# Kernel optimization log

Measured on AMD Instinct MI355X. Metric: run time of the kernel, lower is better.

## Reference

```python
import jax, jax.numpy as jnp
import numpy as np

N = 50000      # nodes
E = 800000     # edges
F_IN = 128     # input_dim
H = 4          # GAT heads
C = 32         # hidden_dim (per head)
HC = H * C     # 128, concat GAT output
NG = 64        # graphs in batch
OUT = 10       # classes


def _gat_conv(x, src, dst, W, att_src, att_dst, bias):
    # PyG GATConv (concat=True, add_self_loops=True, negative_slope=0.2)
    n = x.shape[0]
    h = (x @ W).reshape(n, H, -1)                      # [N,H,C]
    a_s = (h * att_src).sum(-1)                        # [N,H]
    a_d = (h * att_dst).sum(-1)                        # [N,H]
    loop = jnp.arange(n)
    s = jnp.concatenate([src, loop])                   # self-loops appended
    d = jnp.concatenate([dst, loop])
    e = jax.nn.leaky_relu(a_s[s] + a_d[d], 0.2)        # [E+N,H]
    m = jax.ops.segment_max(e, d, num_segments=n)
    e = jnp.exp(e - m[d])
    z = jax.ops.segment_sum(e, d, num_segments=n)
    alpha = e / (z[d] + 1e-16)                         # edge softmax per dst,head
    out = jax.ops.segment_sum(h[s] * alpha[..., None], d, num_segments=n)
    return out.reshape(n, -1) + bias                   # [N,H*C]


def setup_inputs() -> dict:
    key = jax.random.key(0)
    ks = jax.random.split(key, 20)
    g = lambda k, shp, fan: jax.random.normal(k, shp, jnp.float32) / np.sqrt(fan)
    inp = {
        'x': jax.random.normal(ks[0], (N, F_IN), jnp.float32),
        'edge_index': jax.random.randint(ks[1], (2, E), 0, N),
        'batch': jnp.sort(jax.random.randint(ks[2], (N,), 0, NG)),
        # GATConv 1: F_IN -> H*C
        'W1': g(ks[3], (F_IN, HC), F_IN),
        'as1': g(ks[4], (H, C), C), 'ad1': g(ks[5], (H, C), C),
        'b1': jnp.zeros((HC,), jnp.float32),
        # GATConv 2: H*C -> H*C
        'W2': g(ks[6], (HC, HC), HC),
        'as2': g(ks[7], (H, C), C), 'ad2': g(ks[8], (H, C), C),
        'b2': jnp.zeros((HC,), jnp.float32),
        # GraphConv: H*C -> C  (lin_rel has bias, lin_root does not)
        'W3r': g(ks[9], (HC, C), HC), 'W3l': g(ks[10], (HC, C), HC),
        'b3': jnp.zeros((C,), jnp.float32),
        # SAGEConv: C -> C (mean aggr; lin_l has bias, lin_r does not)
        'W4l': g(ks[11], (C, C), C), 'b4l': jnp.zeros((C,), jnp.float32),
        'W4r': g(ks[12], (C, C), C),
        # MLP head
        'Wf1': g(ks[13], (C, C), C), 'bf1': jnp.zeros((C,), jnp.float32),
        'Wf2': g(ks[14], (C, OUT), C), 'bf2': jnp.zeros((OUT,), jnp.float32),
    }
    return inp


def reference(x, edge_index, batch, W1, as1, ad1, b1, W2, as2, ad2, b2,
              W3r, W3l, b3, W4l, b4l, W4r, Wf1, bf1, Wf2, bf2):
    src, dst = edge_index[0], edge_index[1]
    relu = jax.nn.relu
    n = x.shape[0]
    # GAT layers (dropout is identity in eval)
    x = relu(_gat_conv(x, src, dst, W1, as1, ad1, b1))
    x = relu(_gat_conv(x, src, dst, W2, as2, ad2, b2))
    # GraphConv: lin_rel(sum_neighbors) + lin_root(x)
    agg = jax.ops.segment_sum(x[src], dst, num_segments=n)
    x = relu(agg @ W3r + b3 + x @ W3l)
    # SAGEConv: lin_l(mean_neighbors) + lin_r(x)
    deg = jax.ops.segment_sum(jnp.ones((src.shape[0],), x.dtype), dst, num_segments=n)
    mean = jax.ops.segment_sum(x[src], dst, num_segments=n) / jnp.maximum(deg, 1.0)[:, None]
    x = relu(mean @ W4l + b4l + x @ W4r)
    # global mean pool over graphs
    cnt = jax.ops.segment_sum(jnp.ones((n,), x.dtype), batch, num_segments=NG)
    gpool = jax.ops.segment_sum(x, batch, num_segments=NG) / jnp.maximum(cnt, 1.0)[:, None]
    gpool = relu(gpool @ Wf1 + bf1)
    return gpool @ Wf2 + bf2
```

## Files before the change

### kernel.cpp

```cpp
#include <hip/hip_runtime.h>
#include <hip/hip_bf16.h>
#include <type_traits>


typedef __bf16 v8bf __attribute__((ext_vector_type(8)));
typedef float  v4f  __attribute__((ext_vector_type(4)));

__device__ __forceinline__ float lrelu(float x) { return x > 0.f ? x : 0.2f * x; }

__device__ __forceinline__ unsigned short f2bf(float f) {
    unsigned u = __float_as_uint(f);
    unsigned r = (u + 0x7FFF + ((u >> 16) & 1)) >> 16;
    return (unsigned short)r;
}
__device__ __forceinline__ float bfbits2f(unsigned short u) {
    return __uint_as_float((unsigned)u << 16);
}
__device__ __forceinline__ float bflo(int v) { return __uint_as_float((unsigned)v << 16); }
__device__ __forceinline__ float bfhi(int v) { return __uint_as_float((unsigned)v & 0xffff0000u); }
__device__ __forceinline__ int packbf2(float a, float b) {
    return (int)f2bf(a) | ((int)f2bf(b) << 16);
}

__device__ __forceinline__ void fma8(float* acc, int4 u, float w) {
    acc[0] += w * bflo(u.x); acc[1] += w * bfhi(u.x);
    acc[2] += w * bflo(u.y); acc[3] += w * bfhi(u.y);
    acc[4] += w * bflo(u.z); acc[5] += w * bfhi(u.z);
    acc[6] += w * bflo(u.w); acc[7] += w * bfhi(u.w);
}


__global__ __launch_bounds__(256) void bucket_hist(const int* __restrict__ dst,
                                                   int* __restrict__ bcount,
                                                   int E, int nbuck) {
    __shared__ int hist[256];
    int t = threadIdx.x;
    for (int i = t; i < nbuck; i += 256) hist[i] = 0;
    __syncthreads();
    int base = blockIdx.x * 4096;
    #pragma unroll
    for (int k = 0; k < 16; ++k) {
        int e = base + k * 256 + t;
        if (e < E) atomicAdd(&hist[dst[e] >> 8], 1);
    }
    __syncthreads();
    for (int i = t; i < nbuck; i += 256) {
        int c = hist[i];
        if (c) atomicAdd(&bcount[i], c);
    }
}

__global__ __launch_bounds__(256) void scan_convert(
    const int* __restrict__ bcount, int* __restrict__ bbase, int* __restrict__ gcursor,
    int nbuck, int E, int* __restrict__ rowptr, int n,
    const float* __restrict__ W1, const float* __restrict__ W2,
    const float* __restrict__ W3r, const float* __restrict__ W3l,
    const float* __restrict__ as1, const float* __restrict__ ad1,
    const float* __restrict__ as2, const float* __restrict__ ad2,
    __hip_bfloat16* __restrict__ W1t, __hip_bfloat16* __restrict__ W2t,
    __hip_bfloat16* __restrict__ W3rt, __hip_bfloat16* __restrict__ W3lt)
{
    int t = threadIdx.x;
    if (blockIdx.x == 0) {
        __shared__ int red[256];
        int v = (t < nbuck) ? bcount[t] : 0;
        red[t] = v;
        __syncthreads();
        for (int off = 1; off < 256; off <<= 1) {
            int u = (t >= off) ? red[t - off] : 0;
            __syncthreads();
            red[t] += u;
            __syncthreads();
        }
        int ex = red[t] - v;
        if (t < nbuck) { bbase[t] = ex; gcursor[t] = ex; }
        if (t == 0) { bbase[nbuck] = E; rowptr[n] = E; }
        return;
    }
    int b = blockIdx.x - 1;
    int i = b * 256 + t;
    {
        int k = i >> 7, c = i & 127;
        *(unsigned short*)&W1t[c * 128 + k] = f2bf(W1[i]);
        *(unsigned short*)&W2t[c * 128 + k] = f2bf(W2[i]);
    }
    if (i < 4096) {
        int k = i >> 5, c = i & 31;
        *(unsigned short*)&W3rt[c * 128 + k] = f2bf(W3r[i]);
        *(unsigned short*)&W3lt[c * 128 + k] = f2bf(W3l[i]);
    }
    if (b == 0) {
        for (int u = t; u < 512; u += 256) {
            int k = u & 127, hd = u >> 7;
            float vs1 = 0.f, vd1 = 0.f, vs2 = 0.f, vd2 = 0.f;
            #pragma unroll
            for (int j = 0; j < 32; ++j) {
                int c = hd * 32 + j;
                float w1 = W1[k * 128 + c], w2 = W2[k * 128 + c];
                vs1 += w1 * as1[c]; vd1 += w1 * ad1[c];
                vs2 += w2 * as2[c]; vd2 += w2 * ad2[c];
            }
            unsigned short h1s = f2bf(vs1), h1d = f2bf(vd1);
            unsigned short h2s = f2bf(vs2), h2d = f2bf(vd2);
            *(unsigned short*)&W1t[(128 + hd) * 128 + k] = h1s;
            *(unsigned short*)&W1t[(132 + hd) * 128 + k] = f2bf(vs1 - bfbits2f(h1s));
            *(unsigned short*)&W1t[(136 + hd) * 128 + k] = h1d;
            *(unsigned short*)&W1t[(140 + hd) * 128 + k] = f2bf(vd1 - bfbits2f(h1d));
            *(unsigned short*)&W2t[(128 + hd) * 128 + k] = h2s;
            *(unsigned short*)&W2t[(132 + hd) * 128 + k] = f2bf(vs2 - bfbits2f(h2s));
            *(unsigned short*)&W2t[(136 + hd) * 128 + k] = h2d;
            *(unsigned short*)&W2t[(140 + hd) * 128 + k] = f2bf(vd2 - bfbits2f(h2d));
        }
    }
}

__global__ __launch_bounds__(256) void bucket_scatter(const int* __restrict__ dst,
                                                      const int* __restrict__ src,
                                                      int* __restrict__ gcursor,
                                                      int* __restrict__ pairs,
                                                      int E, int nbuck) {
    __shared__ int hist[256], lcur[256];
    int t = threadIdx.x;
    for (int i = t; i < nbuck; i += 256) hist[i] = 0;
    __syncthreads();
    int base = blockIdx.x * 2048;
    int dreg[8];
    #pragma unroll
    for (int k = 0; k < 8; ++k) {
        int e = base + k * 256 + t;
        int d = (e < E) ? dst[e] : -1;
        dreg[k] = d;
        if (d >= 0) atomicAdd(&hist[d >> 8], 1);
    }
    __syncthreads();
    for (int i = t; i < nbuck; i += 256) {
        int c = hist[i];
        lcur[i] = c ? atomicAdd(&gcursor[i], c) : 0;
    }
    __syncthreads();
    #pragma unroll
    for (int k = 0; k < 8; ++k) {
        int e = base + k * 256 + t;
        if (e < E) {
            int d = dreg[k];
            int p = atomicAdd(&lcur[d >> 8], 1);
            pairs[p] = ((d & 255) << 17) | src[e];
        }
    }
}

__global__ __launch_bounds__(256) void bucket_fill(const int* __restrict__ pairs,
                                                   const int* __restrict__ bbase,
                                                   int* __restrict__ rowptr,
                                                   int* __restrict__ colsrc, int n) {
    __shared__ int deg[256], excl[256], cur[256];
    int b = blockIdx.x, t = threadIdx.x;
    int e0 = bbase[b], e1 = bbase[b + 1];
    int d0 = b << 8;
    deg[t] = 0;
    __syncthreads();
    for (int j = e0 + t; j < e1; j += 256)
        atomicAdd(&deg[pairs[j] >> 17], 1);
    __syncthreads();
    int v = deg[t];
    excl[t] = v;
    __syncthreads();
    for (int off = 1; off < 256; off <<= 1) {
        int u = (t >= off) ? excl[t - off] : 0;
        __syncthreads();
        excl[t] += u;
        __syncthreads();
    }
    int base = e0 + excl[t] - v;
    if (d0 + t < n) rowptr[d0 + t] = base;
    cur[t] = base;
    __syncthreads();
    for (int j = e0 + t; j < e1; j += 256) {
        int w = pairs[j];
        int p = atomicAdd(&cur[w >> 17], 1);
        colsrc[p] = w & 0x1FFFF;
    }
}

template <typename T>
__global__ __launch_bounds__(256) void gemm_att_mfma(
    const T* __restrict__ X, const __hip_bfloat16* __restrict__ Wt,
    __hip_bfloat16* __restrict__ h, float* __restrict__ a_s, float* __restrict__ a_d, int n)
{
    __shared__ __align__(16) __hip_bfloat16 sWt[144 * 136];
    int t = threadIdx.x;
    for (int i = t; i < 144 * 16; i += 256) {
        int row = i >> 4, chh = i & 15;
        *(int4*)&sWt[row * 136 + chh * 8] = *(const int4*)&Wt[row * 128 + chh * 8];
    }
    __syncthreads();
    int wave = t >> 6, lane = t & 63, quad = lane >> 4, l16 = lane & 15;

    v8bf z;
    #pragma unroll
    for (int i = 0; i < 8; ++i) z[i] = (__bf16)0.f;

    int nrb = (n + 15) >> 4;
    for (int rb = blockIdx.x * 4 + wave; rb < nrb; rb += gridDim.x * 4) {
        int rowbase = rb * 16;
        int arow = rowbase + l16;
        bool ok = arow < n;
        v8bf af[4];
        if constexpr (std::is_same<T, float>::value) {
            const float* xf = X + (size_t)(ok ? arow : 0) * 128;
            #pragma unroll
            for (int ks = 0; ks < 4; ++ks) {
                if (ok) {
                    float4 u = *(const float4*)&xf[ks * 32 + quad * 8];
                    float4 v = *(const float4*)&xf[ks * 32 + quad * 8 + 4];
                    v8bf a;
                    unsigned short r;
                    r = f2bf(u.x); a[0] = *(__bf16*)&r;
                    r = f2bf(u.y); a[1] = *(__bf16*)&r;
                    r = f2bf(u.z); a[2] = *(__bf16*)&r;
                    r = f2bf(u.w); a[3] = *(__bf16*)&r;
                    r = f2bf(v.x); a[4] = *(__bf16*)&r;
                    r = f2bf(v.y); a[5] = *(__bf16*)&r;
                    r = f2bf(v.z); a[6] = *(__bf16*)&r;
                    r = f2bf(v.w); a[7] = *(__bf16*)&r;
                    af[ks] = a;
                } else af[ks] = z;
            }
        } else {
            const v8bf* px = (const v8bf*)(X + (size_t)(ok ? arow : 0) * 128);
            #pragma unroll
            for (int ks = 0; ks < 4; ++ks) af[ks] = ok ? px[ks * 4 + quad] : z;
        }

        v4f acc[9];
        #pragma unroll
        for (int ct = 0; ct < 9; ++ct) acc[ct] = (v4f){0.f, 0.f, 0.f, 0.f};
        #pragma unroll
        for (int ct = 0; ct < 9; ++ct) {
            #pragma unroll
            for (int ks = 0; ks < 4; ++ks) {
                v8bf b = *(const v8bf*)&sWt[(ct * 16 + l16) * 136 + ks * 32 + quad * 8];
                acc[ct] = __builtin_amdgcn_mfma_f32_16x16x32_bf16(af[ks], b, acc[ct], 0, 0, 0);
            }
        }

        #pragma unroll
        for (int reg = 0; reg < 4; ++reg) {
            int r = rowbase + quad * 4 + reg;
            if (r < n) {
                #pragma unroll
                for (int ct = 0; ct < 8; ++ct)
                    *(unsigned short*)&h[(size_t)r * 128 + ct * 16 + l16] = f2bf(acc[ct][reg]);
            }
        }
        #pragma unroll
        for (int reg = 0; reg < 4; ++reg) {
            float v = acc[8][reg] + __shfl_xor(acc[8][reg], 4);
            int r = rowbase + quad * 4 + reg;
            if (r < n) {
                if (l16 < 4)                    a_s[r * 4 + l16] = v;
                else if (l16 >= 8 && l16 < 12)  a_d[r * 4 + (l16 - 8)] = v;
            }
        }
    }
}

__global__ __launch_bounds__(256) void gat_aggr(
    const __hip_bfloat16* __restrict__ h, const float* __restrict__ a_s,
    const float* __restrict__ a_d,
    const int* __restrict__ rowptr, const int* __restrict__ colsrc,
    const float* __restrict__ bias, __hip_bfloat16* __restrict__ out, int n)
{
    __shared__ float s_w[4][2 * 32 * 4];
    int t = threadIdx.x;
    int wave = t >> 6, lane = t & 63;
    int half = lane >> 5, hl = lane & 31;
    int d = blockIdx.x * 8 + wave * 2 + half;
    if (d >= n) d = n - 1;
    int beg = rowptr[d], end = rowptr[d + 1];
    int cnt = end - beg;
    int cmax = max(cnt, __shfl_xor(cnt, 32));
    float4 ad4 = *(const float4*)&a_d[d * 4];
    float4 asd = *(const float4*)&a_s[d * 4];
    float es0 = lrelu(asd.x + ad4.x), es1 = lrelu(asd.y + ad4.y);
    float es2 = lrelu(asd.z + ad4.z), es3 = lrelu(asd.w + ad4.w);

    int egrp = hl >> 4, l16 = hl & 15;
    int ch = l16 * 8;
    int head = l16 >> 2;
    const char* hb = (const char*)h;
    unsigned chb = (unsigned)(ch << 1);
    int sbase = half * 128;
    int lbase = half * 32;

    float acc[8];
    #pragma unroll
    for (int i = 0; i < 8; ++i) acc[i] = 0.f;
    float zp = 0.f;

    for (int j0 = 0; j0 < cmax; j0 += 32) {
        int ne = cnt - j0;
        float w0 = 0.f, w1 = 0.f, w2 = 0.f, w3 = 0.f;
        int s = 0;
        if (hl < ne) {
            s = colsrc[beg + j0 + hl];
            float4 sv = *(const float4*)&a_s[s * 4];
            w0 = __expf(lrelu(sv.x + ad4.x));
            w1 = __expf(lrelu(sv.y + ad4.y));
            w2 = __expf(lrelu(sv.z + ad4.z));
            w3 = __expf(lrelu(sv.w + ad4.w));
        }
        float4 wv = {w0, w1, w2, w3};
        *(float4*)&s_w[wave][sbase + hl * 4] = wv;
        __asm volatile("s_waitcnt lgkmcnt(0)" ::: "memory");
        int nemax = cmax - j0; if (nemax > 32) nemax = 32;
        int kmax = (nemax + 1) >> 1;
        int k = 0;
        for (; k + 4 <= kmax; k += 4) {
            int jb = egrp + 2 * k;
            int ss0 = __shfl(s, lbase + jb);
            int ss1 = __shfl(s, lbase + jb + 2);
            int ss2 = __shfl(s, lbase + jb + 4);
            int ss3 = __shfl(s, lbase + jb + 6);
            float wj0 = s_w[wave][sbase + jb * 4 + head];
            float wj1 = s_w[wave][sbase + (jb + 2) * 4 + head];
            float wj2 = s_w[wave][sbase + (jb + 4) * 4 + head];
            float wj3 = s_w[wave][sbase + (jb + 6) * 4 + head];
            int4 u0 = *(const int4*)(hb + (((unsigned)ss0 << 8) + chb));
            int4 u1 = *(const int4*)(hb + (((unsigned)ss1 << 8) + chb));
            int4 u2 = *(const int4*)(hb + (((unsigned)ss2 << 8) + chb));
            int4 u3 = *(const int4*)(hb + (((unsigned)ss3 << 8) + chb));
            zp += (wj0 + wj1) + (wj2 + wj3);
            fma8(acc, u0, wj0);
            fma8(acc, u1, wj1);
            fma8(acc, u2, wj2);
            fma8(acc, u3, wj3);
        }
        for (; k + 2 <= kmax; k += 2) {
            int jb = egrp + 2 * k;
            int ss0 = __shfl(s, lbase + jb);
            int ss1 = __shfl(s, lbase + jb + 2);
            float wj0 = s_w[wave][sbase + jb * 4 + head];
            float wj1 = s_w[wave][sbase + (jb + 2) * 4 + head];
            int4 u0 = *(const int4*)(hb + (((unsigned)ss0 << 8) + chb));
            int4 u1 = *(const int4*)(hb + (((unsigned)ss1 << 8) + chb));
            zp += wj0 + wj1;
            fma8(acc, u0, wj0);
            fma8(acc, u1, wj1);
        }
        if (k < kmax) {
            int jb = egrp + 2 * k;
            int ss0 = __shfl(s, lbase + jb);
            float wj0 = s_w[wave][sbase + jb * 4 + head];
            int4 u0 = *(const int4*)(hb + (((unsigned)ss0 << 8) + chb));
            zp += wj0;
            fma8(acc, u0, wj0);
        }
    }

    int4 hu = {0, 0, 0, 0};
    float4 b0 = {0.f, 0.f, 0.f, 0.f}, b1 = {0.f, 0.f, 0.f, 0.f};
    if (egrp == 0) {
        hu = *(const int4*)(hb + (((unsigned)d << 8) + chb));
        b0 = *(const float4*)&bias[ch];
        b1 = *(const float4*)&bias[ch + 4];
    }
    zp += __shfl_xor(zp, 16);
    #pragma unroll
    for (int i = 0; i < 8; ++i) acc[i] += __shfl_xor(acc[i], 16);

    if (egrp == 0) {
        float eh = (head < 2) ? (head == 0 ? es0 : es1) : (head == 2 ? es2 : es3);
        float ws = __expf(eh);
        float inv = 1.f / (zp + ws + 1e-16f);
        float hs[8] = {bflo(hu.x), bfhi(hu.x), bflo(hu.y), bfhi(hu.y),
                       bflo(hu.z), bfhi(hu.z), bflo(hu.w), bfhi(hu.w)};
        float o[8];
        o[0] = fmaxf((acc[0] + ws * hs[0]) * inv + b0.x, 0.f);
        o[1] = fmaxf((acc[1] + ws * hs[1]) * inv + b0.y, 0.f);
        o[2] = fmaxf((acc[2] + ws * hs[2]) * inv + b0.z, 0.f);
        o[3] = fmaxf((acc[3] + ws * hs[3]) * inv + b0.w, 0.f);
        o[4] = fmaxf((acc[4] + ws * hs[4]) * inv + b1.x, 0.f);
        o[5] = fmaxf((acc[5] + ws * hs[5]) * inv + b1.y, 0.f);
        o[6] = fmaxf((acc[6] + ws * hs[6]) * inv + b1.z, 0.f);
        o[7] = fmaxf((acc[7] + ws * hs[7]) * inv + b1.w, 0.f);
        int4 ou;
        ou.x = packbf2(o[0], o[1]); ou.y = packbf2(o[2], o[3]);
        ou.z = packbf2(o[4], o[5]); ou.w = packbf2(o[6], o[7]);
        *(int4*)&out[(size_t)d * 128 + ch] = ou;
    }
}

__global__ __launch_bounds__(256) void graphconv_lin(
    const __hip_bfloat16* __restrict__ Xb,
    const __hip_bfloat16* __restrict__ Wrt, const __hip_bfloat16* __restrict__ Wlt,
    const float* __restrict__ bias, __hip_bfloat16* __restrict__ y,
    float* __restrict__ root, int n)
{
    __shared__ __align__(16) __hip_bfloat16 sWr[32 * 136], sWl[32 * 136];
    int t = threadIdx.x;
    for (int i = t; i < 32 * 16; i += 256) {
        int row = i >> 4, chh = i & 15;
        *(int4*)&sWr[row * 136 + chh * 8] = *(const int4*)&Wrt[row * 128 + chh * 8];
        *(int4*)&sWl[row * 136 + chh * 8] = *(const int4*)&Wlt[row * 128 + chh * 8];
    }
    __syncthreads();
    int wave = t >> 6, lane = t & 63, quad = lane >> 4, l16 = lane & 15;

    v8bf z;
    #pragma unroll
    for (int i = 0; i < 8; ++i) z[i] = (__bf16)0.f;

    int nrb = (n + 15) >> 4;
    for (int rb = blockIdx.x * 4 + wave; rb < nrb; rb += gridDim.x * 4) {
        int rowbase = rb * 16;
        int arow = rowbase + l16;
        bool ok = arow < n;
        const v8bf* px = (const v8bf*)(Xb + (size_t)(ok ? arow : 0) * 128);
        v8bf fx[4];
        #pragma unroll
        for (int ks = 0; ks < 4; ++ks) fx[ks] = ok ? px[ks * 4 + quad] : z;

        v4f accR[2], accL[2];
        #pragma unroll
        for (int ct = 0; ct < 2; ++ct) {
            accR[ct] = (v4f){0.f, 0.f, 0.f, 0.f};
            accL[ct] = (v4f){0.f, 0.f, 0.f, 0.f};
            #pragma unroll
            for (int ks = 0; ks < 4; ++ks) {
                v8bf br = *(const v8bf*)&sWr[(ct * 16 + l16) * 136 + ks * 32 + quad * 8];
                accR[ct] = __builtin_amdgcn_mfma_f32_16x16x32_bf16(fx[ks], br, accR[ct], 0, 0, 0);
                v8bf bl = *(const v8bf*)&sWl[(ct * 16 + l16) * 136 + ks * 32 + quad * 8];
                accL[ct] = __builtin_amdgcn_mfma_f32_16x16x32_bf16(fx[ks], bl, accL[ct], 0, 0, 0);
            }
        }
        #pragma unroll
        for (int ct = 0; ct < 2; ++ct) {
            float bcol = bias[ct * 16 + l16];
            #pragma unroll
            for (int reg = 0; reg < 4; ++reg) {
                int r = rowbase + quad * 4 + reg;
                if (r < n) {
                    *(unsigned short*)&y[(size_t)r * 32 + ct * 16 + l16] = f2bf(accR[ct][reg]);
                    root[(size_t)r * 32 + ct * 16 + l16] = accL[ct][reg] + bcol;
                }
            }
        }
    }
}

__global__ __launch_bounds__(256) void graphconv_aggr(
    const __hip_bfloat16* __restrict__ y, const float* __restrict__ root,
    const int* __restrict__ rowptr, const int* __restrict__ colsrc,
    __hip_bfloat16* __restrict__ x3, int n)
{
    int t = threadIdx.x;
    int wave = t >> 6, lane = t & 63;
    int qr = lane >> 4, hl = lane & 15;
    int d = blockIdx.x * 16 + wave * 4 + qr;
    if (d >= n) d = n - 1;
    int beg = rowptr[d];
    int cnt = rowptr[d + 1] - beg;
    int cm = max(cnt, __shfl_xor(cnt, 16));
    cm = max(cm, __shfl_xor(cm, 32));
    int l4 = hl & 3, egrp = hl >> 2;
    int ch = l4 * 8;
    int lbase = qr * 16;
    float acc[8];
    #pragma unroll
    for (int i = 0; i < 8; ++i) acc[i] = 0.f;
    for (int j0 = 0; j0 < cm; j0 += 16) {
        int ne = cnt - j0;
        int s = (hl < ne) ? colsrc[beg + j0 + hl] : 0;
        int nemax = cm - j0; if (nemax > 16) nemax = 16;
        int kmax = (nemax + 3) >> 2;
        int k = 0;
        for (; k + 2 <= kmax; k += 2) {
            int ja = egrp + 4 * k, jb = ja + 4;
            int sa = __shfl(s, lbase + ja);
            int sb = __shfl(s, lbase + jb);
            float ma = (ja < ne) ? 1.f : 0.f;
            float mb = (jb < ne) ? 1.f : 0.f;
            int4 ua = *(const int4*)&y[(size_t)sa * 32 + ch];
            int4 ub = *(const int4*)&y[(size_t)sb * 32 + ch];
            fma8(acc, ua, ma);
            fma8(acc, ub, mb);
        }
        if (k < kmax) {
            int ja = egrp + 4 * k;
            int sa = __shfl(s, lbase + ja);
            float ma = (ja < ne) ? 1.f : 0.f;
            int4 ua = *(const int4*)&y[(size_t)sa * 32 + ch];
            fma8(acc, ua, ma);
        }
    }
    float4 r0 = {0.f, 0.f, 0.f, 0.f}, r1 = {0.f, 0.f, 0.f, 0.f};
    if (egrp == 0) {
        r0 = *(const float4*)&root[(size_t)d * 32 + ch];
        r1 = *(const float4*)&root[(size_t)d * 32 + ch + 4];
    }
    #pragma unroll
    for (int off = 4; off < 16; off <<= 1)
        #pragma unroll
        for (int i = 0; i < 8; ++i) acc[i] += __shfl_xor(acc[i], off);
    if (egrp == 0) {
        float o[8];
        o[0] = fmaxf(acc[0] + r0.x, 0.f); o[1] = fmaxf(acc[1] + r0.y, 0.f);
        o[2] = fmaxf(acc[2] + r0.z, 0.f); o[3] = fmaxf(acc[3] + r0.w, 0.f);
        o[4] = fmaxf(acc[4] + r1.x, 0.f); o[5] = fmaxf(acc[5] + r1.y, 0.f);
        o[6] = fmaxf(acc[6] + r1.z, 0.f); o[7] = fmaxf(acc[7] + r1.w, 0.f);
        int4 ou;
        ou.x = packbf2(o[0], o[1]); ou.y = packbf2(o[2], o[3]);
        ou.z = packbf2(o[4], o[5]); ou.w = packbf2(o[6], o[7]);
        *(int4*)&x3[(size_t)d * 32 + ch] = ou;
    }
}

__global__ __launch_bounds__(256) void mean_aggr32(
    const __hip_bfloat16* __restrict__ x, const int* __restrict__ rowptr,
    const int* __restrict__ colsrc, float* __restrict__ mean, int n)
{
    int t = threadIdx.x;
    int wave = t >> 6, lane = t & 63;
    int qr = lane >> 4, hl = lane & 15;
    int d = blockIdx.x * 16 + wave * 4 + qr;
    if (d >= n) d = n - 1;
    int beg = rowptr[d];
    int cnt = rowptr[d + 1] - beg;
    int cm = max(cnt, __shfl_xor(cnt, 16));
    cm = max(cm, __shfl_xor(cm, 32));
    int l4 = hl & 3, egrp = hl >> 2;
    int ch = l4 * 8;
    int lbase = qr * 16;
    float acc[8];
    #pragma unroll
    for (int i = 0; i < 8; ++i) acc[i] = 0.f;
    for (int j0 = 0; j0 < cm; j0 += 16) {
        int ne = cnt - j0;
        int s = (hl < ne) ? colsrc[beg + j0 + hl] : 0;
        int nemax = cm - j0; if (nemax > 16) nemax = 16;
        int kmax = (nemax + 3) >> 2;
        int k = 0;
        for (; k + 2 <= kmax; k += 2) {
            int ja = egrp + 4 * k, jb = ja + 4;
            int sa = __shfl(s, lbase + ja);
            int sb = __shfl(s, lbase + jb);
            float ma = (ja < ne) ? 1.f : 0.f;
            float mb = (jb < ne) ? 1.f : 0.f;
            int4 ua = *(const int4*)&x[(size_t)sa * 32 + ch];
            int4 ub = *(const int4*)&x[(size_t)sb * 32 + ch];
            fma8(acc, ua, ma);
            fma8(acc, ub, mb);
        }
        if (k < kmax) {
            int ja = egrp + 4 * k;
            int sa = __shfl(s, lbase + ja);
            float ma = (ja < ne) ? 1.f : 0.f;
            int4 ua = *(const int4*)&x[(size_t)sa * 32 + ch];
            fma8(acc, ua, ma);
        }
    }
    #pragma unroll
    for (int off = 4; off < 16; off <<= 1)
        #pragma unroll
        for (int i = 0; i < 8; ++i) acc[i] += __shfl_xor(acc[i], off);
    if (egrp == 0) {
        float invd = 1.f / fmaxf((float)cnt, 1.f);
        float4 lo = {acc[0] * invd, acc[1] * invd, acc[2] * invd, acc[3] * invd};
        float4 hi = {acc[4] * invd, acc[5] * invd, acc[6] * invd, acc[7] * invd};
        *(float4*)&mean[(size_t)d * 32 + ch]     = lo;
        *(float4*)&mean[(size_t)d * 32 + ch + 4] = hi;
    }
}

__global__ __launch_bounds__(256) void sage_gemm(
    const float* __restrict__ mean, const __hip_bfloat16* __restrict__ xin,
    const float* __restrict__ Wl, const float* __restrict__ bl,
    const float* __restrict__ Wr, float* __restrict__ out, int n)
{
    __shared__ __align__(16) float sWl[32 * 32], sWr[32 * 32];
    __shared__ __align__(16) float sm[8 * 32], sx[8 * 32];
    int t = threadIdx.x;
    for (int i = t; i < 1024; i += 256) { sWl[i] = Wl[i]; sWr[i] = Wr[i]; }
    int c = t & 31, rr = t >> 5;
    float bc = bl[c];
    for (int row0 = blockIdx.x * 8; row0 < n; row0 += gridDim.x * 8) {
        __syncthreads();
        {
            int i = t;
            int r = i >> 5, cc = i & 31;
            int row = row0 + r;
            sm[i] = (row < n) ? mean[row * 32 + cc] : 0.f;
            sx[i] = (row < n) ? bfbits2f(*(const unsigned short*)&xin[row * 32 + cc]) : 0.f;
        }
        __syncthreads();
        float acc = bc;
        const float4* pm = (const float4*)&sm[rr * 32];
        const float4* px = (const float4*)&sx[rr * 32];
        #pragma unroll
        for (int k4 = 0; k4 < 8; ++k4) {
            float4 vm = pm[k4], vx = px[k4];
            const float* wl = &sWl[(k4 * 4) * 32 + c];
            const float* wr = &sWr[(k4 * 4) * 32 + c];
            acc += vm.x * wl[0] + vm.y * wl[32] + vm.z * wl[64] + vm.w * wl[96];
            acc += vx.x * wr[0] + vx.y * wr[32] + vx.z * wr[64] + vx.w * wr[96];
        }
        int row = row0 + rr;
        if (row < n) out[row * 32 + c] = fmaxf(acc, 0.f);
    }
}

__device__ __forceinline__ int lower_bound_i(const int* a, int n, int key) {
    int lo = 0, hi = n;
    while (lo < hi) { int mid = (lo + hi) >> 1; if (a[mid] < key) lo = mid + 1; else hi = mid; }
    return lo;
}

__global__ __launch_bounds__(256) void pool_kernel(
    const float* __restrict__ x, const int* __restrict__ batch,
    float* __restrict__ gpool, int n)
{
    int g = blockIdx.x;
    int lo = lower_bound_i(batch, n, g);
    int hi = lower_bound_i(batch, n, g + 1);
    int t = threadIdx.x;
    int c = t & 31, rr = t >> 5;
    float acc = 0.f;
    for (int i = lo + rr; i < hi; i += 8) acc += x[i * 32 + c];
    __shared__ float sred[256];
    sred[t] = acc;
    __syncthreads();
    if (t < 128) sred[t] += sred[t + 128];
    __syncthreads();
    if (t < 64) sred[t] += sred[t + 64];
    __syncthreads();
    if (t < 32) {
        float v = sred[t] + sred[t + 32];
        gpool[g * 32 + t] = v / fmaxf((float)(hi - lo), 1.f);
    }
}

__global__ __launch_bounds__(256) void head_kernel(
    const float* __restrict__ gpool, const float* __restrict__ Wf1, const float* __restrict__ bf1,
    const float* __restrict__ Wf2, const float* __restrict__ bf2, float* __restrict__ out)
{
    __shared__ float sg[64 * 32], st[64 * 32];
    __shared__ float sW1[32 * 32], sW2[32 * 10];
    int t = threadIdx.x;
    for (int i = t; i < 2048; i += 256) sg[i] = gpool[i];
    for (int i = t; i < 1024; i += 256) sW1[i] = Wf1[i];
    for (int i = t; i < 320; i += 256) sW2[i] = Wf2[i];
    __syncthreads();
    for (int i = t; i < 2048; i += 256) {
        int g = i >> 5, c = i & 31;
        float acc = bf1[c];
        #pragma unroll
        for (int k = 0; k < 32; ++k) acc += sg[g * 32 + k] * sW1[k * 32 + c];
        st[i] = fmaxf(acc, 0.f);
    }
    __syncthreads();
    for (int i = t; i < 640; i += 256) {
        int g = i / 10, o = i - g * 10;
        float acc = bf2[o];
        #pragma unroll
        for (int k = 0; k < 32; ++k) acc += st[g * 32 + k] * sW2[k * 10 + o];
        out[i] = acc;
    }
}

extern "C" void kernel_launch(void* const* d_in, const int* in_sizes, int n_in,
                              void* d_out, int out_size, void* d_ws, size_t ws_size,
                              hipStream_t stream) {
    const float* x    = (const float*)d_in[0];
    const int*   ei   = (const int*)d_in[1];
    const int*   batch= (const int*)d_in[2];
    const float* W1   = (const float*)d_in[3];
    const float* as1  = (const float*)d_in[4];
    const float* ad1  = (const float*)d_in[5];
    const float* b1   = (const float*)d_in[6];
    const float* W2   = (const float*)d_in[7];
    const float* as2  = (const float*)d_in[8];
    const float* ad2  = (const float*)d_in[9];
    const float* b2   = (const float*)d_in[10];
    const float* W3r  = (const float*)d_in[11];
    const float* W3l  = (const float*)d_in[12];
    const float* b3   = (const float*)d_in[13];
    const float* W4l  = (const float*)d_in[14];
    const float* b4l  = (const float*)d_in[15];
    const float* W4r  = (const float*)d_in[16];
    const float* Wf1  = (const float*)d_in[17];
    const float* bf1  = (const float*)d_in[18];
    const float* Wf2  = (const float*)d_in[19];
    const float* bf2  = (const float*)d_in[20];

    const int N = in_sizes[0] / 128;
    const int E = in_sizes[1] / 2;
    const int* src = ei;
    const int* dst = ei + E;

    char* p = (char*)d_ws;
    auto alloc = [&](size_t bytes) -> void* {
        void* r = (void*)p;
        p += (bytes + 255) & ~(size_t)255;
        return r;
    };
    __hip_bfloat16* buf1 = (__hip_bfloat16*)alloc((size_t)N * 128 * 2);
    __hip_bfloat16* buf2 = (__hip_bfloat16*)alloc((size_t)N * 128 * 2);
    __hip_bfloat16* buf3 = (__hip_bfloat16*)alloc((size_t)N * 128 * 2);
    float* aS     = (float*)alloc((size_t)N * 4 * 4);
    float* aD     = (float*)alloc((size_t)N * 4 * 4);
    int*   rowptr = (int*)alloc((size_t)(N + 1) * 4);
    int*   colsrc = (int*)alloc((size_t)E * 4);
    int*   bcount = (int*)alloc(256 * 4);
    int*   bbase  = (int*)alloc(257 * 4);
    int*   gcursor= (int*)alloc(256 * 4);
    __hip_bfloat16* W1t  = (__hip_bfloat16*)alloc(144 * 128 * 2);
    __hip_bfloat16* W2t  = (__hip_bfloat16*)alloc(144 * 128 * 2);
    __hip_bfloat16* W3rt = (__hip_bfloat16*)alloc(32 * 128 * 2);
    __hip_bfloat16* W3lt = (__hip_bfloat16*)alloc(32 * 128 * 2);
    float* gpool  = (float*)alloc(64 * 32 * 4);

    __hip_bfloat16* X3b  = buf2;
    float*          MEAN = (float*)((char*)buf2 + (((size_t)N * 32 * 2 + 255) & ~(size_t)255));
    float*          X4   = (float*)buf1;
    __hip_bfloat16* Y32  = buf3;
    float*          ROOT = (float*)((char*)buf3 + (((size_t)N * 32 * 2 + 255) & ~(size_t)255));
    int*            pairs = (int*)buf3;

    const int nbuck = (N + 255) >> 8;

    hipMemsetAsync(bcount, 0, 256 * 4, stream);
    bucket_hist<<<(E + 4095) / 4096, 256, 0, stream>>>(dst, bcount, E, nbuck);
    scan_convert<<<65, 256, 0, stream>>>(bcount, bbase, gcursor, nbuck, E, rowptr, N,
                                         W1, W2, W3r, W3l, as1, ad1, as2, ad2,
                                         W1t, W2t, W3rt, W3lt);
    bucket_scatter<<<(E + 2047) / 2048, 256, 0, stream>>>(dst, src, gcursor, pairs, E, nbuck);
    bucket_fill<<<nbuck, 256, 0, stream>>>(pairs, bbase, rowptr, colsrc, N);

    int gmm = (N + 63) / 64;
    if (gmm > 320) gmm = 320;
    const int gag2 = (N + 7) / 8;
    const int gag4 = (N + 15) / 16;
    gemm_att_mfma<float><<<gmm, 256, 0, stream>>>(x, W1t, buf3, aS, aD, N);
    gat_aggr<<<gag2, 256, 0, stream>>>(buf3, aS, aD, rowptr, colsrc, b1, buf2, N);
    gemm_att_mfma<__hip_bfloat16><<<gmm, 256, 0, stream>>>(buf2, W2t, buf3, aS, aD, N);
    gat_aggr<<<gag2, 256, 0, stream>>>(buf3, aS, aD, rowptr, colsrc, b2, buf1, N);
    graphconv_lin<<<gmm, 256, 0, stream>>>(buf1, W3rt, W3lt, b3, Y32, ROOT, N);
    graphconv_aggr<<<gag4, 256, 0, stream>>>(Y32, ROOT, rowptr, colsrc, X3b, N);
    mean_aggr32<<<gag4, 256, 0, stream>>>(X3b, rowptr, colsrc, MEAN, N);
    sage_gemm<<<1024, 256, 0, stream>>>(MEAN, X3b, W4l, b4l, W4r, X4, N);
    pool_kernel<<<64, 256, 0, stream>>>(X4, batch, gpool, N);
    head_kernel<<<1, 256, 0, stream>>>(gpool, Wf1, bf1, Wf2, bf2, (float*)d_out);
}
```

Measured before the change: 328.9 us.

## Narrow per-node lane groups in GAT and 32-wide aggregation kernels

The GAT aggregation now gives each destination node 16 lanes instead of 32, so one wave handles four nodes and there is no cross-group reduction at the end. The graphconv and mean aggregation kernels give each node 8 lanes instead of 16, so one wave handles eight nodes with a single shuffle reduction. Both changes aim to cut idle lanes and shuffle-reduction overhead on low-degree nodes (average degree about 16). In exchange, each lane serialises more edges per node, so there is less memory-level parallelism per node and more divergence from degree imbalance within a wave.

```diff
diff --git a/kernel.cpp b/kernel.cpp
--- a/kernel.cpp
+++ b/kernel.cpp
@@ -271,39 +271,37 @@
     const int* __restrict__ rowptr, const int* __restrict__ colsrc,
     const float* __restrict__ bias, __hip_bfloat16* __restrict__ out, int n)
 {
-    __shared__ float s_w[4][2 * 32 * 4];
+    __shared__ float s_w[4][4 * 16 * 4];
     int t = threadIdx.x;
     int wave = t >> 6, lane = t & 63;
-    int half = lane >> 5, hl = lane & 31;
-    int d = blockIdx.x * 8 + wave * 2 + half;
+    int q = lane >> 4, l16 = lane & 15;
+    int d = blockIdx.x * 16 + wave * 4 + q;
     if (d >= n) d = n - 1;
-    int beg = rowptr[d], end = rowptr[d + 1];
-    int cnt = end - beg;
-    int cmax = max(cnt, __shfl_xor(cnt, 32));
+    int beg = rowptr[d];
+    int cnt = rowptr[d + 1] - beg;
+    int cm = max(cnt, __shfl_xor(cnt, 16));
+    cm = max(cm, __shfl_xor(cm, 32));
     float4 ad4 = *(const float4*)&a_d[d * 4];
     float4 asd = *(const float4*)&a_s[d * 4];
-    float es0 = lrelu(asd.x + ad4.x), es1 = lrelu(asd.y + ad4.y);
-    float es2 = lrelu(asd.z + ad4.z), es3 = lrelu(asd.w + ad4.w);
-
-    int egrp = hl >> 4, l16 = hl & 15;
+
     int ch = l16 * 8;
     int head = l16 >> 2;
     const char* hb = (const char*)h;
     unsigned chb = (unsigned)(ch << 1);
-    int sbase = half * 128;
-    int lbase = half * 32;
+    int sbase = q * 64;
+    int lbase = q * 16;
 
     float acc[8];
     #pragma unroll
     for (int i = 0; i < 8; ++i) acc[i] = 0.f;
     float zp = 0.f;
 
-    for (int j0 = 0; j0 < cmax; j0 += 32) {
+    for (int j0 = 0; j0 < cm; j0 += 16) {
         int ne = cnt - j0;
         float w0 = 0.f, w1 = 0.f, w2 = 0.f, w3 = 0.f;
         int s = 0;
-        if (hl < ne) {
-            s = colsrc[beg + j0 + hl];
+        if (l16 < ne) {
+            s = colsrc[beg + j0 + l16];
             float4 sv = *(const float4*)&a_s[s * 4];
             w0 = __expf(lrelu(sv.x + ad4.x));
             w1 = __expf(lrelu(sv.y + ad4.y));
@@ -311,21 +309,19 @@
             w3 = __expf(lrelu(sv.w + ad4.w));
         }
         float4 wv = {w0, w1, w2, w3};
-        *(float4*)&s_w[wave][sbase + hl * 4] = wv;
+        *(float4*)&s_w[wave][sbase + l16 * 4] = wv;
         __asm volatile("s_waitcnt lgkmcnt(0)" ::: "memory");
-        int nemax = cmax - j0; if (nemax > 32) nemax = 32;
-        int kmax = (nemax + 1) >> 1;
+        int nemax = cm - j0; if (nemax > 16) nemax = 16;
         int k = 0;
-        for (; k + 4 <= kmax; k += 4) {
-            int jb = egrp + 2 * k;
-            int ss0 = __shfl(s, lbase + jb);
-            int ss1 = __shfl(s, lbase + jb + 2);
-            int ss2 = __shfl(s, lbase + jb + 4);
-            int ss3 = __shfl(s, lbase + jb + 6);
-            float wj0 = s_w[wave][sbase + jb * 4 + head];
-            float wj1 = s_w[wave][sbase + (jb + 2) * 4 + head];
-            float wj2 = s_w[wave][sbase + (jb + 4) * 4 + head];
-            float wj3 = s_w[wave][sbase + (jb + 6) * 4 + head];
+        for (; k + 4 <= nemax; k += 4) {
+            int ss0 = __shfl(s, lbase + k);
+            int ss1 = __shfl(s, lbase + k + 1);
+            int ss2 = __shfl(s, lbase + k + 2);
+            int ss3 = __shfl(s, lbase + k + 3);
+            float wj0 = s_w[wave][sbase + k * 4 + head];
+            float wj1 = s_w[wave][sbase + (k + 1) * 4 + head];
+            float wj2 = s_w[wave][sbase + (k + 2) * 4 + head];
+            float wj3 = s_w[wave][sbase + (k + 3) * 4 + head];
             int4 u0 = *(const int4*)(hb + (((unsigned)ss0 << 8) + chb));
             int4 u1 = *(const int4*)(hb + (((unsigned)ss1 << 8) + chb));
             int4 u2 = *(const int4*)(hb + (((unsigned)ss2 << 8) + chb));
@@ -336,59 +332,38 @@
             fma8(acc, u2, wj2);
             fma8(acc, u3, wj3);
         }
-        for (; k + 2 <= kmax; k += 2) {
-            int jb = egrp + 2 * k;
-            int ss0 = __shfl(s, lbase + jb);
-            int ss1 = __shfl(s, lbase + jb + 2);
-            float wj0 = s_w[wave][sbase + jb * 4 + head];
-            float wj1 = s_w[wave][sbase + (jb + 2) * 4 + head];
-            int4 u0 = *(const int4*)(hb + (((unsigned)ss0 << 8) + chb));
-            int4 u1 = *(const int4*)(hb + (((unsigned)ss1 << 8) + chb));
-            zp += wj0 + wj1;
-            fma8(acc, u0, wj0);
-            fma8(acc, u1, wj1);
-        }
-        if (k < kmax) {
-            int jb = egrp + 2 * k;
-            int ss0 = __shfl(s, lbase + jb);
-            float wj0 = s_w[wave][sbase + jb * 4 + head];
+        for (; k < nemax; ++k) {
+            int ss0 = __shfl(s, lbase + k);
+            float wj0 = s_w[wave][sbase + k * 4 + head];
             int4 u0 = *(const int4*)(hb + (((unsigned)ss0 << 8) + chb));
             zp += wj0;
             fma8(acc, u0, wj0);
         }
     }
 
-    int4 hu = {0, 0, 0, 0};
-    float4 b0 = {0.f, 0.f, 0.f, 0.f}, b1 = {0.f, 0.f, 0.f, 0.f};
-    if (egrp == 0) {
-        hu = *(const int4*)(hb + (((unsigned)d << 8) + chb));
-        b0 = *(const float4*)&bias[ch];
-        b1 = *(const float4*)&bias[ch + 4];
-    }
-    zp += __shfl_xor(zp, 16);
-    #pragma unroll
-    for (int i = 0; i < 8; ++i) acc[i] += __shfl_xor(acc[i], 16);
-
-    if (egrp == 0) {
-        float eh = (head < 2) ? (head == 0 ? es0 : es1) : (head == 2 ? es2 : es3);
-        float ws = __expf(eh);
-        float inv = 1.f / (zp + ws + 1e-16f);
-        float hs[8] = {bflo(hu.x), bfhi(hu.x), bflo(hu.y), bfhi(hu.y),
-                       bflo(hu.z), bfhi(hu.z), bflo(hu.w), bfhi(hu.w)};
-        float o[8];
-        o[0] = fmaxf((acc[0] + ws * hs[0]) * inv + b0.x, 0.f);
-        o[1] = fmaxf((acc[1] + ws * hs[1]) * inv + b0.y, 0.f);
-        o[2] = fmaxf((acc[2] + ws * hs[2]) * inv + b0.z, 0.f);
-        o[3] = fmaxf((acc[3] + ws * hs[3]) * inv + b0.w, 0.f);
-        o[4] = fmaxf((acc[4] + ws * hs[4]) * inv + b1.x, 0.f);
-        o[5] = fmaxf((acc[5] + ws * hs[5]) * inv + b1.y, 0.f);
-        o[6] = fmaxf((acc[6] + ws * hs[6]) * inv + b1.z, 0.f);
-        o[7] = fmaxf((acc[7] + ws * hs[7]) * inv + b1.w, 0.f);
-        int4 ou;
-        ou.x = packbf2(o[0], o[1]); ou.y = packbf2(o[2], o[3]);
-        ou.z = packbf2(o[4], o[5]); ou.w = packbf2(o[6], o[7]);
-        *(int4*)&out[(size_t)d * 128 + ch] = ou;
-    }
+    int4 hu = *(const int4*)(hb + (((unsigned)d << 8) + chb));
+    float4 b0 = *(const float4*)&bias[ch];
+    float4 b1 = *(const float4*)&bias[ch + 4];
+    float eh0 = lrelu(asd.x + ad4.x), eh1 = lrelu(asd.y + ad4.y);
+    float eh2 = lrelu(asd.z + ad4.z), eh3 = lrelu(asd.w + ad4.w);
+    float eh = (head < 2) ? (head == 0 ? eh0 : eh1) : (head == 2 ? eh2 : eh3);
+    float ws = __expf(eh);
+    float inv = 1.f / (zp + ws + 1e-16f);
+    float hs[8] = {bflo(hu.x), bfhi(hu.x), bflo(hu.y), bfhi(hu.y),
+                   bflo(hu.z), bfhi(hu.z), bflo(hu.w), bfhi(hu.w)};
+    float o[8];
+    o[0] = fmaxf((acc[0] + ws * hs[0]) * inv + b0.x, 0.f);
+    o[1] = fmaxf((acc[1] + ws * hs[1]) * inv + b0.y, 0.f);
+    o[2] = fmaxf((acc[2] + ws * hs[2]) * inv + b0.z, 0.f);
+    o[3] = fmaxf((acc[3] + ws * hs[3]) * inv + b0.w, 0.f);
+    o[4] = fmaxf((acc[4] + ws * hs[4]) * inv + b1.x, 0.f);
+    o[5] = fmaxf((acc[5] + ws * hs[5]) * inv + b1.y, 0.f);
+    o[6] = fmaxf((acc[6] + ws * hs[6]) * inv + b1.z, 0.f);
+    o[7] = fmaxf((acc[7] + ws * hs[7]) * inv + b1.w, 0.f);
+    int4 ou;
+    ou.x = packbf2(o[0], o[1]); ou.y = packbf2(o[2], o[3]);
+    ou.z = packbf2(o[4], o[5]); ou.w = packbf2(o[6], o[7]);
+    *(int4*)&out[(size_t)d * 128 + ch] = ou;
 }
 
 __global__ __launch_bounds__(256) void graphconv_lin(
@@ -456,27 +431,28 @@
 {
     int t = threadIdx.x;
     int wave = t >> 6, lane = t & 63;
-    int qr = lane >> 4, hl = lane & 15;
-    int d = blockIdx.x * 16 + wave * 4 + qr;
+    int oct = lane >> 3, ol = lane & 7;
+    int d = blockIdx.x * 32 + wave * 8 + oct;
     if (d >= n) d = n - 1;
     int beg = rowptr[d];
     int cnt = rowptr[d + 1] - beg;
-    int cm = max(cnt, __shfl_xor(cnt, 16));
+    int cm = max(cnt, __shfl_xor(cnt, 8));
+    cm = max(cm, __shfl_xor(cm, 16));
     cm = max(cm, __shfl_xor(cm, 32));
-    int l4 = hl & 3, egrp = hl >> 2;
+    int l4 = ol & 3, egrp = ol >> 2;
     int ch = l4 * 8;
-    int lbase = qr * 16;
+    int lbase = oct * 8;
     float acc[8];
     #pragma unroll
     for (int i = 0; i < 8; ++i) acc[i] = 0.f;
-    for (int j0 = 0; j0 < cm; j0 += 16) {
+    for (int j0 = 0; j0 < cm; j0 += 8) {
         int ne = cnt - j0;
-        int s = (hl < ne) ? colsrc[beg + j0 + hl] : 0;
-        int nemax = cm - j0; if (nemax > 16) nemax = 16;
-        int kmax = (nemax + 3) >> 2;
+        int s = (ol < ne) ? colsrc[beg + j0 + ol] : 0;
+        int nemax = cm - j0; if (nemax > 8) nemax = 8;
+        int kmax = (nemax + 1) >> 1;
         int k = 0;
         for (; k + 2 <= kmax; k += 2) {
-            int ja = egrp + 4 * k, jb = ja + 4;
+            int ja = egrp + 2 * k, jb = ja + 2;
             int sa = __shfl(s, lbase + ja);
             int sb = __shfl(s, lbase + jb);
             float ma = (ja < ne) ? 1.f : 0.f;
@@ -487,7 +463,7 @@
             fma8(acc, ub, mb);
         }
         if (k < kmax) {
-            int ja = egrp + 4 * k;
+            int ja = egrp + 2 * k;
             int sa = __shfl(s, lbase + ja);
             float ma = (ja < ne) ? 1.f : 0.f;
             int4 ua = *(const int4*)&y[(size_t)sa * 32 + ch];
@@ -500,9 +476,7 @@
         r1 = *(const float4*)&root[(size_t)d * 32 + ch + 4];
     }
     #pragma unroll
-    for (int off = 4; off < 16; off <<= 1)
-        #pragma unroll
-        for (int i = 0; i < 8; ++i) acc[i] += __shfl_xor(acc[i], off);
+    for (int i = 0; i < 8; ++i) acc[i] += __shfl_xor(acc[i], 4);
     if (egrp == 0) {
         float o[8];
         o[0] = fmaxf(acc[0] + r0.x, 0.f); o[1] = fmaxf(acc[1] + r0.y, 0.f);
@@ -522,27 +496,28 @@
 {
     int t = threadIdx.x;
     int wave = t >> 6, lane = t & 63;
-    int qr = lane >> 4, hl = lane & 15;
-    int d = blockIdx.x * 16 + wave * 4 + qr;
+    int oct = lane >> 3, ol = lane & 7;
+    int d = blockIdx.x * 32 + wave * 8 + oct;
     if (d >= n) d = n - 1;
     int beg = rowptr[d];
     int cnt = rowptr[d + 1] - beg;
-    int cm = max(cnt, __shfl_xor(cnt, 16));
+    int cm = max(cnt, __shfl_xor(cnt, 8));
+    cm = max(cm, __shfl_xor(cm, 16));
     cm = max(cm, __shfl_xor(cm, 32));
-    int l4 = hl & 3, egrp = hl >> 2;
+    int l4 = ol & 3, egrp = ol >> 2;
     int ch = l4 * 8;
-    int lbase = qr * 16;
+    int lbase = oct * 8;
     float acc[8];
     #pragma unroll
     for (int i = 0; i < 8; ++i) acc[i] = 0.f;
-    for (int j0 = 0; j0 < cm; j0 += 16) {
+    for (int j0 = 0; j0 < cm; j0 += 8) {
         int ne = cnt - j0;
-        int s = (hl < ne) ? colsrc[beg + j0 + hl] : 0;
-        int nemax = cm - j0; if (nemax > 16) nemax = 16;
-        int kmax = (nemax + 3) >> 2;
+        int s = (ol < ne) ? colsrc[beg + j0 + ol] : 0;
+        int nemax = cm - j0; if (nemax > 8) nemax = 8;
+        int kmax = (nemax + 1) >> 1;
         int k = 0;
         for (; k + 2 <= kmax; k += 2) {
-            int ja = egrp + 4 * k, jb = ja + 4;
+            int ja = egrp + 2 * k, jb = ja + 2;
             int sa = __shfl(s, lbase + ja);
             int sb = __shfl(s, lbase + jb);
             float ma = (ja < ne) ? 1.f : 0.f;
@@ -553,7 +528,7 @@
             fma8(acc, ub, mb);
         }
         if (k < kmax) {
-            int ja = egrp + 4 * k;
+            int ja = egrp + 2 * k;
             int sa = __shfl(s, lbase + ja);
             float ma = (ja < ne) ? 1.f : 0.f;
             int4 ua = *(const int4*)&x[(size_t)sa * 32 + ch];
@@ -561,9 +536,7 @@
         }
     }
     #pragma unroll
-    for (int off = 4; off < 16; off <<= 1)
-        #pragma unroll
-        for (int i = 0; i < 8; ++i) acc[i] += __shfl_xor(acc[i], off);
+    for (int i = 0; i < 8; ++i) acc[i] += __shfl_xor(acc[i], 4);
     if (egrp == 0) {
         float invd = 1.f / fmaxf((float)cnt, 1.f);
         float4 lo = {acc[0] * invd, acc[1] * invd, acc[2] * invd, acc[3] * invd};
@@ -739,15 +712,15 @@
 
     int gmm = (N + 63) / 64;
     if (gmm > 320) gmm = 320;
-    const int gag2 = (N + 7) / 8;
-    const int gag4 = (N + 15) / 16;
+    const int gag4  = (N + 15) / 16;
+    const int gag8  = (N + 31) / 32;
     gemm_att_mfma<float><<<gmm, 256, 0, stream>>>(x, W1t, buf3, aS, aD, N);
-    gat_aggr<<<gag2, 256, 0, stream>>>(buf3, aS, aD, rowptr, colsrc, b1, buf2, N);
+    gat_aggr<<<gag4, 256, 0, stream>>>(buf3, aS, aD, rowptr, colsrc, b1, buf2, N);
     gemm_att_mfma<__hip_bfloat16><<<gmm, 256, 0, stream>>>(buf2, W2t, buf3, aS, aD, N);
-    gat_aggr<<<gag2, 256, 0, stream>>>(buf3, aS, aD, rowptr, colsrc, b2, buf1, N);
+    gat_aggr<<<gag4, 256, 0, stream>>>(buf3, aS, aD, rowptr, colsrc, b2, buf1, N);
     graphconv_lin<<<gmm, 256, 0, stream>>>(buf1, W3rt, W3lt, b3, Y32, ROOT, N);
-    graphconv_aggr<<<gag4, 256, 0, stream>>>(Y32, ROOT, rowptr, colsrc, X3b, N);
-    mean_aggr32<<<gag4, 256, 0, stream>>>(X3b, rowptr, colsrc, MEAN, N);
+    graphconv_aggr<<<gag8, 256, 0, stream>>>(Y32, ROOT, rowptr, colsrc, X3b, N);
+    mean_aggr32<<<gag8, 256, 0, stream>>>(X3b, rowptr, colsrc, MEAN, N);
     sage_gemm<<<1024, 256, 0, stream>>>(MEAN, X3b, W4l, b4l, W4r, X4, N);
     pool_kernel<<<64, 256, 0, stream>>>(X4, batch, gpool, N);
     head_kernel<<<1, 256, 0, stream>>>(gpool, Wf1, bf1, Wf2, bf2, (float*)d_out);
```

After: 327.9 us. About the same (-0.3%).
